# Kernel optimization log

Measured on AMD Instinct MI355X. Metric: run time of the kernel, lower is better.

Reference implementation:

```python
import jax, jax.numpy as jnp
import numpy as np

K = 3        # kernel_size
STRIDE = 1
PAD = 1


def _conv2d(x, w, stride, pad):
    return jax.lax.conv_general_dilated(
        x, w, window_strides=(stride, stride),
        padding=((pad, pad), (pad, pad)),
        dimension_numbers=("NCHW", "OIHW", "NCHW"))


def setup_inputs() -> dict:
    key = jax.random.key(0)
    k1, k2, k3, k4 = jax.random.split(key, 4)
    B, C, H, W = 8, 128, 56, 56
    OUT = 128
    x = jax.random.normal(k1, (B, C, H, W), jnp.float32)
    # small offset weights keep sampled coords mostly in-bounds (realistic trained regime)
    offset_w = jax.random.normal(k2, (2 * K * K, C, K, K), jnp.float32) * 0.01
    offset_b = jax.random.normal(k3, (2 * K * K,), jnp.float32) * 0.01
    conv_w = jax.random.normal(k4, (OUT, C, K, K), jnp.float32) * 0.02
    return {"x": x, "offset_w": offset_w, "offset_b": offset_b, "conv_w": conv_w}


def reference(x, offset_w, offset_b, conv_w):
    n = K * K
    # offset prediction conv (stride=STRIDE, padding=k//2) -> [b, 2n, h, w]
    offset = _conv2d(x, offset_w, STRIDE, K // 2) + offset_b[None, :, None, None]
    b, _, h, w = offset.shape
    # zero padding of the feature map
    xp = jnp.pad(x, ((0, 0), (0, 0), (PAD, PAD), (PAD, PAD)))
    c, Hp, Wp = xp.shape[1], xp.shape[2], xp.shape[3]

    # pn: fixed kernel offsets, y-first then x (matches torch.cat(y.flatten(), x.flatten()))
    r = jnp.arange(-(K // 2), K // 2 + 1, dtype=jnp.float32)
    py_n, px_n = jnp.meshgrid(r, r, indexing="ij")
    pn = jnp.concatenate([py_n.ravel(), px_n.ravel()])          # (2n,)

    # p0: kernel-center coordinates in padded map
    gy = jnp.arange(K // 2, h * STRIDE + 1, STRIDE, dtype=jnp.float32)
    gx = jnp.arange(K // 2, w * STRIDE + 1, STRIDE, dtype=jnp.float32)
    p0y, p0x = jnp.meshgrid(gy, gx, indexing="ij")               # (h, w)
    p0 = jnp.concatenate([jnp.broadcast_to(p0y, (n, h, w)),
                          jnp.broadcast_to(p0x, (n, h, w))], axis=0)[None]  # (1, 2n, h, w)

    p = p0 + pn[None, :, None, None] + offset                    # (b, 2n, h, w)
    p = jnp.transpose(p, (0, 2, 3, 1))                           # (b, h, w, 2n)

    q = jax.lax.stop_gradient(jnp.floor(p))                      # p.detach().floor()
    qlt_y = jnp.clip(q[..., :n], 0, Hp - 1)
    qlt_x = jnp.clip(q[..., n:], 0, Wp - 1)
    qrb_y = jnp.clip(q[..., :n] + 1, 0, Hp - 1)
    qrb_x = jnp.clip(q[..., n:] + 1, 0, Wp - 1)
    py = jnp.clip(p[..., :n], 0, Hp - 1)
    px = jnp.clip(p[..., n:], 0, Wp - 1)

    # bilinear weights; jnp.trunc reproduces the original's .long() truncation on one factor
    g_lt = (1 - (py - qlt_y)) * jnp.trunc(1 - (px - qlt_x))
    g_rb = (1 - (qrb_y - py)) * jnp.trunc(1 - (qrb_x - px))
    g_lb = (1 - (py - qlt_y)) * (1 - (qrb_x - px))               # q_lb = (qlt_y, qrb_x)
    g_rt = (1 - (qrb_y - py)) * (1 - (px - qlt_x))               # q_rt = (qrb_y, qlt_x)

    x_flat = xp.reshape(b, c, Hp * Wp)

    def gather(qy, qx):
        idx = (qy * Wp + qx).astype(jnp.int32).reshape(b, 1, -1)  # (b,1,h*w*n)
        out = jnp.take_along_axis(x_flat, jnp.broadcast_to(idx, (b, c, idx.shape[-1])), axis=-1)
        return out.reshape(b, c, h, w, n)

    x_off = (g_lt[:, None] * gather(qlt_y, qlt_x)
             + g_rb[:, None] * gather(qrb_y, qrb_x)
             + g_lb[:, None] * gather(qlt_y, qrb_x)
             + g_rt[:, None] * gather(qrb_y, qlt_x))             # (b, c, h, w, n)

    # tile each kxk sampled patch into a (h*k, w*k) map, matching _reshape_x_offset
    x_off = x_off.reshape(b, c, h, w, K, K).transpose(0, 1, 2, 4, 3, 5).reshape(b, c, h * K, w * K)

    # final conv: kernel k, stride k, no padding -> (b, out, h, w)
    return _conv2d(x_off, conv_w, K, 0)
```

## Files before the change

### kernel.cpp

```cpp
#include <hip/hip_runtime.h>
#include <cstdint>
#include <cstddef>

namespace {

constexpr int Bn   = 8;
constexpr int Cc   = 128;
constexpr int Hh   = 56;
constexpr int Ww   = 56;
constexpr int OUTC = 128;
constexpr int NTAP = 9;
constexpr int HW   = 3136;
constexpr int NPOS = Bn * HW;
constexpr int KDIM = 1152;
constexpr int CH   = Bn * 18 * HW;

constexpr int PT   = 32;
constexpr int CCH  = 64;
constexpr int KC   = CCH * NTAP;
constexpr int LROW = 584;

constexpr int OFFBLK = 1568;
constexpr int WBLK   = 576;

typedef __attribute__((ext_vector_type(8))) short  short8v;
typedef __attribute__((ext_vector_type(4))) short  short4v;
typedef __attribute__((ext_vector_type(4))) float  float4v;

__device__ __forceinline__ unsigned short f2bf(float f) {
    union { float f; uint32_t u; } v; v.f = f;
    const uint32_t u = v.u;
    return (unsigned short)((u + 0x7fffu + ((u >> 16) & 1u)) >> 16);
}
__device__ __forceinline__ float bf2f(unsigned short us) {
    union { uint32_t u; float f; } v; v.u = (uint32_t)us << 16;
    return v.f;
}

__global__ __launch_bounds__(256) void fused_prep_offset_kernel(
        const float* __restrict__ x, const float* __restrict__ ow,
        const float* __restrict__ cw,
        unsigned short* __restrict__ cwb, unsigned short* __restrict__ xt,
        float* __restrict__ partial) {
    __shared__ float red[4][64 * 18];

    const int blk = blockIdx.x;
    const int t   = threadIdx.x;

    if (blk >= OFFBLK) {
        const int pb = blk - OFFBLK;
        if (pb < WBLK) {
            const int i = pb * 256 + t;
            const int u   = i & 7;
            const int mq  = (i >> 3) & 63;
            const int wvv = (i >> 9) & 7;
            const int rest = i >> 12;
            const int ks = rest % 18, ccg = rest / 18;
            const int mm = mq >> 2, quad = mq & 3;
            const int klocal = ks * 32 + quad * 8 + u;
            const int n = klocal >> 6, cl = klocal & 63;
            const int o = wvv * 16 + mm;
            cwb[i] = f2bf(cw[o * KDIM + (ccg * CCH + cl) * NTAP + n]);
            return;
        }
        const int pb2 = pb - WBLK;
        const int b = pb2 & 7;
        const int ijb = (pb2 >> 3) * 64;
        const int lp2 = t & 63, cg = t >> 6;
        const float* xb = x + (size_t)b * Cc * HW + ijb + lp2;
#pragma unroll
        for (int c8 = 0; c8 < 4; ++c8) {
            short8v sv;
#pragma unroll
            for (int u = 0; u < 8; ++u)
                sv[u] = (short)f2bf(xb[(size_t)(cg * 32 + c8 * 8 + u) * HW]);
            const int g16 = cg * 4 + c8;
            *(short8v*)(xt + ((size_t)(b * 16 + g16) * HW + ijb + lp2) * 8) = sv;
        }
        return;
    }

    const int lane = t & 63;
    const int sq   = __builtin_amdgcn_readfirstlane(t >> 6);
    const int chunk = blk & 3;
    const int pgi  = blk >> 2;
    const int b    = pgi & 7;
    const int ijb  = (pgi >> 3) * 64;
    const int ij   = ijb + lane;
    const int i    = ij / Ww, j = ij % Ww;
    const float* xb = x + (size_t)b * Cc * HW;

    float acc[18];
#pragma unroll
    for (int m = 0; m < 18; ++m) acc[m] = 0.f;

    const int c0 = chunk * 32 + sq * 8;
    for (int cc = 0; cc < 8; ++cc) {
        const int c = c0 + cc;
        const float* xc = xb + (size_t)c * HW;
        float xv[9];
#pragma unroll
        for (int ky = 0; ky < 3; ++ky) {
            const int y = i + ky - 1;
            const bool yv = (unsigned)y < (unsigned)Hh;
#pragma unroll
            for (int kx = 0; kx < 3; ++kx) {
                const int xx = j + kx - 1;
                xv[ky * 3 + kx] = (yv && (unsigned)xx < (unsigned)Ww) ? xc[y * Ww + xx] : 0.f;
            }
        }
        const float* wc = ow + c * NTAP;
#pragma unroll
        for (int m = 0; m < 18; ++m) {
#pragma unroll
            for (int tap = 0; tap < 9; ++tap)
                acc[m] = fmaf(wc[m * KDIM + tap], xv[tap], acc[m]);
        }
    }

#pragma unroll
    for (int m = 0; m < 18; ++m) red[sq][lane * 18 + m] = acc[m];
    __syncthreads();

    float* pout = partial + (size_t)chunk * CH;
    for (int e = t; e < 64 * 18; e += 256) {
        const int lpe = e / 18, m = e % 18;
        const float s01 = red[0][e] + red[1][e];
        const float s23 = red[2][e] + red[3][e];
        pout[(size_t)(b * 18 + m) * HW + ijb + lpe] = s01 + s23;
    }
}

__global__ __launch_bounds__(512, 6) void deform_mfma_kernel(
        const unsigned short* __restrict__ xt, const unsigned short* __restrict__ cwb,
        const float* __restrict__ partial, const float* __restrict__ ob,
        float* __restrict__ out) {
    __shared__ unsigned short xoffB[PT * LROW];
    __shared__ float4v pgS[PT * NTAP];
    __shared__ int2    poS[PT * NTAP];

    const int t    = threadIdx.x;
    const int lane = t & 63;
    const int mm   = lane & 15, quad = lane >> 4;
    const int wv   = t >> 6;
    const int lp   = t & 31;
    const int grp  = (t >> 5) & 7;
    const int nh   = t >> 8;
    const int blk  = blockIdx.x;
    const int b    = blk & 7;
    const int ijb  = (blk >> 3) * PT;
    const unsigned short* xtb = xt + (size_t)b * 16 * HW * 8;

    for (int e = t; e < PT * NTAP; e += 512) {
        const int n = e >> 5, lpe = e & 31;
        const int ij = ijb + lpe;
        const size_t iy = (size_t)(b * 18 + n) * HW + ij;
        const size_t ix = (size_t)(b * 18 + 9 + n) * HW + ij;
        float sy = (partial[iy] + partial[CH + iy]) + (partial[2 * CH + iy] + partial[3 * CH + iy]);
        float sx = (partial[ix] + partial[CH + ix]) + (partial[2 * CH + ix] + partial[3 * CH + ix]);
        sy = sy + ob[n];
        sx = sx + ob[9 + n];
        const float py = (float)(ij / Ww + n / 3) + sy;
        const float px = (float)(ij % Ww + n % 3) + sx;
        const float q0y = floorf(py), q0x = floorf(px);
        const float lty = fminf(fmaxf(q0y, 0.f), 57.f);
        const float ltx = fminf(fmaxf(q0x, 0.f), 57.f);
        const float rby = fminf(fmaxf(q0y + 1.f, 0.f), 57.f);
        const float rbx = fminf(fmaxf(q0x + 1.f, 0.f), 57.f);
        const float pyc = fminf(fmaxf(py, 0.f), 57.f);
        const float pxc = fminf(fmaxf(px, 0.f), 57.f);
        float g0 = (1.f - (pyc - lty)) * truncf(1.f - (pxc - ltx));
        float g1 = (1.f - (rby - pyc)) * truncf(1.f - (rbx - pxc));
        float g2 = (1.f - (pyc - lty)) * (1.f - (rbx - pxc));
        float g3 = (1.f - (rby - pyc)) * (1.f - (pxc - ltx));
        const int y0 = (int)lty - 1, x0 = (int)ltx - 1;
        const int y1 = (int)rby - 1, x1 = (int)rbx - 1;
        const bool v0y = (unsigned)y0 < (unsigned)Hh, v0x = (unsigned)x0 < (unsigned)Ww;
        const bool v1y = (unsigned)y1 < (unsigned)Hh, v1x = (unsigned)x1 < (unsigned)Ww;
        int o0 = y0 * Ww + x0, o1 = y1 * Ww + x1, o2 = y0 * Ww + x1, o3 = y1 * Ww + x0;
        if (!(v0y && v0x)) { o0 = 0; g0 = 0.f; }
        if (!(v1y && v1x)) { o1 = 0; g1 = 0.f; }
        if (!(v0y && v1x)) { o2 = 0; g2 = 0.f; }
        if (!(v1y && v0x)) { o3 = 0; g3 = 0.f; }
        pgS[e] = (float4v){ g2, g3, g0, g1 };
        poS[e] = make_int2((o2 & 0xffff) | (o3 << 16), (o0 & 0xffff) | (o1 << 16));
    }

    float4v acc[2] = { {0.f,0.f,0.f,0.f}, {0.f,0.f,0.f,0.f} };
    __syncthreads();

    for (int cc = 0; cc < 2; ++cc) {
        if (cc) __syncthreads();
        const unsigned short* pl = xtb + (size_t)(cc * 8 + grp) * HW * 8;
#pragma unroll
        for (int nn = 0; nn < 5; ++nn) {
            const int n = nn * 2 + nh;
            if (n < 9) {
                const float4v G = pgS[n * 32 + lp];
                const int2  O = poS[n * 32 + lp];
                const short8v a0 = *(const short8v*)(pl + (size_t)(O.y & 0xffff) * 8);
                const short8v a2 = *(const short8v*)(pl + (size_t)(O.x & 0xffff) * 8);
                const short8v a3 = *(const short8v*)(pl + (size_t)((O.x >> 16) & 0xffff) * 8);
                const short8v a1 = *(const short8v*)(pl + (size_t)((O.y >> 16) & 0xffff) * 8);
                short8v sv;
#pragma unroll
                for (int u = 0; u < 8; ++u) {
                    float v = G.x * bf2f((unsigned short)a2[u]);
                    v = fmaf(G.y, bf2f((unsigned short)a3[u]), v);
                    v = fmaf(G.z, bf2f((unsigned short)a0[u]), v);
                    v = fmaf(G.w, bf2f((unsigned short)a1[u]), v);
                    sv[u] = (short)f2bf(v);
                }
                *(short8v*)&xoffB[lp * LROW + n * CCH + grp * 8] = sv;
            }
        }
        __syncthreads();

        const unsigned short* bw = cwb + (size_t)(cc * 144 + wv) * 512 + (mm * 4 + quad) * 8;
        const unsigned short* ap0 = &xoffB[mm * LROW + quad * 8];
#pragma unroll 3
        for (int ks = 0; ks < KC / 32; ++ks) {
            const int kl = ks * 32;
            const short8v b0 = *(const short8v*)(bw + ks * 4096);
#pragma unroll
            for (int pt = 0; pt < 2; ++pt) {
                const unsigned short* ap = ap0 + pt * 16 * LROW + kl;
                const short4v alo = *(const short4v*)ap;
                const short4v ahi = *(const short4v*)(ap + 4);
                const short8v a = __builtin_shufflevector(alo, ahi, 0, 1, 2, 3, 4, 5, 6, 7);
                acc[pt] = __builtin_amdgcn_mfma_f32_16x16x32_bf16(a, b0, acc[pt], 0, 0, 0);
            }
        }
    }

    float* ob0 = out + (size_t)(b * OUTC + wv * 16 + mm) * HW + ijb + quad * 4;
#pragma unroll
    for (int pt = 0; pt < 2; ++pt)
        *(float4v*)(ob0 + pt * 16) = acc[pt];
}

}

extern "C" void kernel_launch(void* const* d_in, const int* in_sizes, int n_in,
                              void* d_out, int out_size, void* d_ws, size_t ws_size,
                              hipStream_t stream) {
    const float* x  = (const float*)d_in[0];
    const float* ow = (const float*)d_in[1];
    const float* ob = (const float*)d_in[2];
    const float* cw = (const float*)d_in[3];
    float* out = (float*)d_out;

    char* wsp = (char*)d_ws;
    unsigned short* cwb = (unsigned short*)wsp;
    unsigned short* xt = (unsigned short*)(wsp + 294912);
    float* partial = (float*)(wsp + 6717440);

    fused_prep_offset_kernel<<<OFFBLK + WBLK + 392, 256, 0, stream>>>(
        x, ow, cw, cwb, xt, partial);
    deform_mfma_kernel<<<NPOS / PT, 512, 0, stream>>>(xt, cwb, partial, ob, out);
}
```

Measured before the change: 127.8 us.

## Merge prep and deform kernels into one persistent cooperative kernel with grid sync

Replaces the two launches with a single cooperative persistent kernel. Each 512-thread block processes two 256-thread prep units per round (offset conv partials, weight bf16 repack, x transpose), then all blocks meet at a grid-wide sync before looping over the deform/MFMA output tiles. The goal is to remove the second launch and the gap between kernels. In exchange it adds a grid barrier, shared-memory aliasing, fewer resident blocks (grid capped at 768) and a redundant duplicate store of each output tile.

```diff
diff --git a/kernel.cpp b/kernel.cpp
--- a/kernel.cpp
+++ b/kernel.cpp
@@ -1,6 +1,9 @@
 #include <hip/hip_runtime.h>
+#include <hip/hip_cooperative_groups.h>
 #include <cstdint>
 #include <cstddef>
+
+namespace cg = cooperative_groups;
 
 namespace {
 
@@ -15,13 +18,15 @@
 constexpr int KDIM = 1152;
 constexpr int CH   = Bn * 18 * HW;
 
-constexpr int PT   = 32;
-constexpr int CCH  = 64;
-constexpr int KC   = CCH * NTAP;
-constexpr int LROW = 584;
+constexpr int PT    = 32;
+constexpr int CCH   = 64;
+constexpr int KC    = CCH * NTAP;
+constexpr int LROW  = 584;
+constexpr int NTILE = NPOS / PT;
 
 constexpr int OFFBLK = 1568;
 constexpr int WBLK   = 576;
+constexpr int NUNIT  = 2536;
 
 typedef __attribute__((ext_vector_type(8))) short  short8v;
 typedef __attribute__((ext_vector_type(4))) short  short4v;
@@ -37,206 +42,222 @@
     return v.f;
 }
 
-__global__ __launch_bounds__(256) void fused_prep_offset_kernel(
+__global__ __launch_bounds__(512, 6) void deform_all(
         const float* __restrict__ x, const float* __restrict__ ow,
-        const float* __restrict__ cw,
+        const float* __restrict__ ob, const float* __restrict__ cw,
         unsigned short* __restrict__ cwb, unsigned short* __restrict__ xt,
-        float* __restrict__ partial) {
-    __shared__ float red[4][64 * 18];
-
+        float* __restrict__ partial, float* __restrict__ out) {
+    __shared__ __align__(16) char smem[44288];
+    const int t   = threadIdx.x;
     const int blk = blockIdx.x;
-    const int t   = threadIdx.x;
-
-    if (blk >= OFFBLK) {
-        const int pb = blk - OFFBLK;
-        if (pb < WBLK) {
-            const int i = pb * 256 + t;
-            const int u   = i & 7;
-            const int mq  = (i >> 3) & 63;
-            const int wvv = (i >> 9) & 7;
-            const int rest = i >> 12;
-            const int ks = rest % 18, ccg = rest / 18;
-            const int mm = mq >> 2, quad = mq & 3;
-            const int klocal = ks * 32 + quad * 8 + u;
-            const int n = klocal >> 6, cl = klocal & 63;
-            const int o = wvv * 16 + mm;
-            cwb[i] = f2bf(cw[o * KDIM + (ccg * CCH + cl) * NTAP + n]);
-            return;
-        }
-        const int pb2 = pb - WBLK;
-        const int b = pb2 & 7;
-        const int ijb = (pb2 >> 3) * 64;
-        const int lp2 = t & 63, cg = t >> 6;
-        const float* xb = x + (size_t)b * Cc * HW + ijb + lp2;
-#pragma unroll
-        for (int c8 = 0; c8 < 4; ++c8) {
-            short8v sv;
-#pragma unroll
-            for (int u = 0; u < 8; ++u)
-                sv[u] = (short)f2bf(xb[(size_t)(cg * 32 + c8 * 8 + u) * HW]);
-            const int g16 = cg * 4 + c8;
-            *(short8v*)(xt + ((size_t)(b * 16 + g16) * HW + ijb + lp2) * 8) = sv;
-        }
-        return;
+    const int g   = gridDim.x;
+
+    {
+        const int h  = t >> 8;
+        const int t2 = t & 255;
+        float* redh = (float*)smem + h * 4608;
+        const int slots  = g * 2;
+        const int rounds = (NUNIT + slots - 1) / slots;
+        for (int r = 0; r < rounds; ++r) {
+            const int vu = r * slots + 2 * blk + h;
+            const bool isoff = (vu < OFFBLK);
+            if (isoff) {
+                const int lane = t2 & 63;
+                const int sq   = __builtin_amdgcn_readfirstlane(t2 >> 6);
+                const int chunk = vu & 3;
+                const int pgi  = vu >> 2;
+                const int b    = pgi & 7;
+                const int ijb  = (pgi >> 3) * 64;
+                const int ij   = ijb + lane;
+                const int i    = ij / Ww, j = ij % Ww;
+                const float* xb = x + (size_t)b * Cc * HW;
+                float acc[18];
+#pragma unroll
+                for (int m = 0; m < 18; ++m) acc[m] = 0.f;
+                const int c0 = chunk * 32 + sq * 8;
+                for (int ccl = 0; ccl < 8; ++ccl) {
+                    const int c = c0 + ccl;
+                    const float* xc = xb + (size_t)c * HW;
+                    float xv[9];
+#pragma unroll
+                    for (int ky = 0; ky < 3; ++ky) {
+                        const int y = i + ky - 1;
+                        const bool yv = (unsigned)y < (unsigned)Hh;
+#pragma unroll
+                        for (int kx = 0; kx < 3; ++kx) {
+                            const int xx = j + kx - 1;
+                            xv[ky * 3 + kx] = (yv && (unsigned)xx < (unsigned)Ww) ? xc[y * Ww + xx] : 0.f;
+                        }
+                    }
+                    const float* wc = ow + c * NTAP;
+#pragma unroll
+                    for (int m = 0; m < 18; ++m) {
+#pragma unroll
+                        for (int tap = 0; tap < 9; ++tap)
+                            acc[m] = fmaf(wc[m * KDIM + tap], xv[tap], acc[m]);
+                    }
+                }
+#pragma unroll
+                for (int m = 0; m < 18; ++m) redh[sq * 1152 + lane * 18 + m] = acc[m];
+            } else if (vu < OFFBLK + WBLK) {
+                const int i = (vu - OFFBLK) * 256 + t2;
+                const int u   = i & 7;
+                const int mq  = (i >> 3) & 63;
+                const int wvv = (i >> 9) & 7;
+                const int rest = i >> 12;
+                const int ks = rest % 18, ccg = rest / 18;
+                const int mmw = mq >> 2, quadw = mq & 3;
+                const int klocal = ks * 32 + quadw * 8 + u;
+                const int n = klocal >> 6, cl = klocal & 63;
+                const int o = wvv * 16 + mmw;
+                cwb[i] = f2bf(cw[o * KDIM + (ccg * CCH + cl) * NTAP + n]);
+            } else if (vu < NUNIT) {
+                const int pb2 = vu - (OFFBLK + WBLK);
+                const int b = pb2 & 7;
+                const int ijb = (pb2 >> 3) * 64;
+                const int lp2 = t2 & 63, cgi = t2 >> 6;
+                const float* xb = x + (size_t)b * Cc * HW + ijb + lp2;
+#pragma unroll
+                for (int c8 = 0; c8 < 4; ++c8) {
+                    short8v sv;
+#pragma unroll
+                    for (int u = 0; u < 8; ++u)
+                        sv[u] = (short)f2bf(xb[(size_t)(cgi * 32 + c8 * 8 + u) * HW]);
+                    const int g16 = cgi * 4 + c8;
+                    *(short8v*)(xt + ((size_t)(b * 16 + g16) * HW + ijb + lp2) * 8) = sv;
+                }
+            }
+            __syncthreads();
+            if (isoff) {
+                const int chunk = vu & 3;
+                const int pgi = vu >> 2;
+                const int b = pgi & 7;
+                const int ijb = (pgi >> 3) * 64;
+                float* pout = partial + (size_t)chunk * CH;
+                for (int e = t2; e < 1152; e += 256) {
+                    const int lpe = e / 18, m = e % 18;
+                    const float s01 = redh[e] + redh[1152 + e];
+                    const float s23 = redh[2304 + e] + redh[3456 + e];
+                    pout[(size_t)(b * 18 + m) * HW + ijb + lpe] = s01 + s23;
+                }
+            }
+            __syncthreads();
+        }
     }
 
-    const int lane = t & 63;
-    const int sq   = __builtin_amdgcn_readfirstlane(t >> 6);
-    const int chunk = blk & 3;
-    const int pgi  = blk >> 2;
-    const int b    = pgi & 7;
-    const int ijb  = (pgi >> 3) * 64;
-    const int ij   = ijb + lane;
-    const int i    = ij / Ww, j = ij % Ww;
-    const float* xb = x + (size_t)b * Cc * HW;
-
-    float acc[18];
-#pragma unroll
-    for (int m = 0; m < 18; ++m) acc[m] = 0.f;
-
-    const int c0 = chunk * 32 + sq * 8;
-    for (int cc = 0; cc < 8; ++cc) {
-        const int c = c0 + cc;
-        const float* xc = xb + (size_t)c * HW;
-        float xv[9];
-#pragma unroll
-        for (int ky = 0; ky < 3; ++ky) {
-            const int y = i + ky - 1;
-            const bool yv = (unsigned)y < (unsigned)Hh;
-#pragma unroll
-            for (int kx = 0; kx < 3; ++kx) {
-                const int xx = j + kx - 1;
-                xv[ky * 3 + kx] = (yv && (unsigned)xx < (unsigned)Ww) ? xc[y * Ww + xx] : 0.f;
-            }
-        }
-        const float* wc = ow + c * NTAP;
-#pragma unroll
-        for (int m = 0; m < 18; ++m) {
-#pragma unroll
-            for (int tap = 0; tap < 9; ++tap)
-                acc[m] = fmaf(wc[m * KDIM + tap], xv[tap], acc[m]);
-        }
-    }
-
-#pragma unroll
-    for (int m = 0; m < 18; ++m) red[sq][lane * 18 + m] = acc[m];
-    __syncthreads();
-
-    float* pout = partial + (size_t)chunk * CH;
-    for (int e = t; e < 64 * 18; e += 256) {
-        const int lpe = e / 18, m = e % 18;
-        const float s01 = red[0][e] + red[1][e];
-        const float s23 = red[2][e] + red[3][e];
-        pout[(size_t)(b * 18 + m) * HW + ijb + lpe] = s01 + s23;
-    }
-}
-
-__global__ __launch_bounds__(512, 6) void deform_mfma_kernel(
-        const unsigned short* __restrict__ xt, const unsigned short* __restrict__ cwb,
-        const float* __restrict__ partial, const float* __restrict__ ob,
-        float* __restrict__ out) {
-    __shared__ unsigned short xoffB[PT * LROW];
-    __shared__ float4v pgS[PT * NTAP];
-    __shared__ int2    poS[PT * NTAP];
-
-    const int t    = threadIdx.x;
+    __threadfence();
+    cg::this_grid().sync();
+
+    unsigned short* xoffB = (unsigned short*)smem;
+    float4v* pgS = (float4v*)(smem + 37376);
+    int2*    poS = (int2*)(smem + 37376 + 4608);
+
     const int lane = t & 63;
     const int mm   = lane & 15, quad = lane >> 4;
     const int wv   = t >> 6;
     const int lp   = t & 31;
     const int grp  = (t >> 5) & 7;
     const int nh   = t >> 8;
-    const int blk  = blockIdx.x;
-    const int b    = blk & 7;
-    const int ijb  = (blk >> 3) * PT;
-    const unsigned short* xtb = xt + (size_t)b * 16 * HW * 8;
-
-    for (int e = t; e < PT * NTAP; e += 512) {
-        const int n = e >> 5, lpe = e & 31;
-        const int ij = ijb + lpe;
-        const size_t iy = (size_t)(b * 18 + n) * HW + ij;
-        const size_t ix = (size_t)(b * 18 + 9 + n) * HW + ij;
-        float sy = (partial[iy] + partial[CH + iy]) + (partial[2 * CH + iy] + partial[3 * CH + iy]);
-        float sx = (partial[ix] + partial[CH + ix]) + (partial[2 * CH + ix] + partial[3 * CH + ix]);
-        sy = sy + ob[n];
-        sx = sx + ob[9 + n];
-        const float py = (float)(ij / Ww + n / 3) + sy;
-        const float px = (float)(ij % Ww + n % 3) + sx;
-        const float q0y = floorf(py), q0x = floorf(px);
-        const float lty = fminf(fmaxf(q0y, 0.f), 57.f);
-        const float ltx = fminf(fmaxf(q0x, 0.f), 57.f);
-        const float rby = fminf(fmaxf(q0y + 1.f, 0.f), 57.f);
-        const float rbx = fminf(fmaxf(q0x + 1.f, 0.f), 57.f);
-        const float pyc = fminf(fmaxf(py, 0.f), 57.f);
-        const float pxc = fminf(fmaxf(px, 0.f), 57.f);
-        float g0 = (1.f - (pyc - lty)) * truncf(1.f - (pxc - ltx));
-        float g1 = (1.f - (rby - pyc)) * truncf(1.f - (rbx - pxc));
-        float g2 = (1.f - (pyc - lty)) * (1.f - (rbx - pxc));
-        float g3 = (1.f - (rby - pyc)) * (1.f - (pxc - ltx));
-        const int y0 = (int)lty - 1, x0 = (int)ltx - 1;
-        const int y1 = (int)rby - 1, x1 = (int)rbx - 1;
-        const bool v0y = (unsigned)y0 < (unsigned)Hh, v0x = (unsigned)x0 < (unsigned)Ww;
-        const bool v1y = (unsigned)y1 < (unsigned)Hh, v1x = (unsigned)x1 < (unsigned)Ww;
-        int o0 = y0 * Ww + x0, o1 = y1 * Ww + x1, o2 = y0 * Ww + x1, o3 = y1 * Ww + x0;
-        if (!(v0y && v0x)) { o0 = 0; g0 = 0.f; }
-        if (!(v1y && v1x)) { o1 = 0; g1 = 0.f; }
-        if (!(v0y && v1x)) { o2 = 0; g2 = 0.f; }
-        if (!(v1y && v0x)) { o3 = 0; g3 = 0.f; }
-        pgS[e] = (float4v){ g2, g3, g0, g1 };
-        poS[e] = make_int2((o2 & 0xffff) | (o3 << 16), (o0 & 0xffff) | (o1 << 16));
+    const unsigned short* xtB = xt;
+
+    for (int base = 0; base < NTILE; base += g) {
+        const int w = (NTILE - base < g) ? (NTILE - base) : g;
+        const int off = blk - (g - w);
+        if (off < 0) continue;
+        const int ti  = base + off;
+        const int b   = ti & 7;
+        const int ijb = (ti >> 3) * PT;
+        const unsigned short* xtb = xtB + (size_t)b * 16 * HW * 8;
+
+        for (int e = t; e < PT * NTAP; e += 512) {
+            const int n = e >> 5, lpe = e & 31;
+            const int ij = ijb + lpe;
+            const size_t iy = (size_t)(b * 18 + n) * HW + ij;
+            const size_t ix = (size_t)(b * 18 + 9 + n) * HW + ij;
+            float sy = (partial[iy] + partial[CH + iy]) + (partial[2 * CH + iy] + partial[3 * CH + iy]);
+            float sx = (partial[ix] + partial[CH + ix]) + (partial[2 * CH + ix] + partial[3 * CH + ix]);
+            sy = sy + ob[n];
+            sx = sx + ob[9 + n];
+            const float py = (float)(ij / Ww + n / 3) + sy;
+            const float px = (float)(ij % Ww + n % 3) + sx;
+            const float q0y = floorf(py), q0x = floorf(px);
+            const float lty = fminf(fmaxf(q0y, 0.f), 57.f);
+            const float ltx = fminf(fmaxf(q0x, 0.f), 57.f);
+            const float rby = fminf(fmaxf(q0y + 1.f, 0.f), 57.f);
+            const float rbx = fminf(fmaxf(q0x + 1.f, 0.f), 57.f);
+            const float pyc = fminf(fmaxf(py, 0.f), 57.f);
+            const float pxc = fminf(fmaxf(px, 0.f), 57.f);
+            float g0 = (1.f - (pyc - lty)) * truncf(1.f - (pxc - ltx));
+            float g1 = (1.f - (rby - pyc)) * truncf(1.f - (rbx - pxc));
+            float g2 = (1.f - (pyc - lty)) * (1.f - (rbx - pxc));
+            float g3 = (1.f - (rby - pyc)) * (1.f - (pxc - ltx));
+            const int y0 = (int)lty - 1, x0 = (int)ltx - 1;
+            const int y1 = (int)rby - 1, x1 = (int)rbx - 1;
+            const bool v0y = (unsigned)y0 < (unsigned)Hh, v0x = (unsigned)x0 < (unsigned)Ww;
+            const bool v1y = (unsigned)y1 < (unsigned)Hh, v1x = (unsigned)x1 < (unsigned)Ww;
+            int o0 = y0 * Ww + x0, o1 = y1 * Ww + x1, o2 = y0 * Ww + x1, o3 = y1 * Ww + x0;
+            if (!(v0y && v0x)) { o0 = 0; g0 = 0.f; }
+            if (!(v1y && v1x)) { o1 = 0; g1 = 0.f; }
+            if (!(v0y && v1x)) { o2 = 0; g2 = 0.f; }
+            if (!(v1y && v0x)) { o3 = 0; g3 = 0.f; }
+            pgS[e] = (float4v){ g2, g3, g0, g1 };
+            poS[e] = make_int2((o2 & 0xffff) | (o3 << 16), (o0 & 0xffff) | (o1 << 16));
+        }
+
+        float4v acc[2] = { {0.f,0.f,0.f,0.f}, {0.f,0.f,0.f,0.f} };
+        __syncthreads();
+
+        for (int cc = 0; cc < 2; ++cc) {
+            if (cc) __syncthreads();
+            const unsigned short* pl = xtb + (size_t)(cc * 8 + grp) * HW * 8;
+#pragma unroll
+            for (int nn = 0; nn < 5; ++nn) {
+                const int n = nn * 2 + nh;
+                if (n < 9) {
+                    const float4v G = pgS[n * 32 + lp];
+                    const int2  O = poS[n * 32 + lp];
+                    const short8v a0 = *(const short8v*)(pl + (size_t)(O.y & 0xffff) * 8);
+                    const short8v a2 = *(const short8v*)(pl + (size_t)(O.x & 0xffff) * 8);
+                    const short8v a3 = *(const short8v*)(pl + (size_t)((O.x >> 16) & 0xffff) * 8);
+                    const short8v a1 = *(const short8v*)(pl + (size_t)((O.y >> 16) & 0xffff) * 8);
+                    short8v sv;
+#pragma unroll
+                    for (int u = 0; u < 8; ++u) {
+                        float v = G.x * bf2f((unsigned short)a2[u]);
+                        v = fmaf(G.y, bf2f((unsigned short)a3[u]), v);
+                        v = fmaf(G.z, bf2f((unsigned short)a0[u]), v);
+                        v = fmaf(G.w, bf2f((unsigned short)a1[u]), v);
+                        sv[u] = (short)f2bf(v);
+                    }
+                    *(short8v*)&xoffB[lp * LROW + n * CCH + grp * 8] = sv;
+                }
+            }
+            __syncthreads();
+
+            const unsigned short* bw = cwb + (size_t)(cc * 144 + wv) * 512 + (mm * 4 + quad) * 8;
+            const unsigned short* ap0 = &xoffB[mm * LROW + quad * 8];
+#pragma unroll 3
+            for (int ks = 0; ks < KC / 32; ++ks) {
+                const int kl = ks * 32;
+                const short8v b0 = *(const short8v*)(bw + ks * 4096);
+#pragma unroll
+                for (int pt = 0; pt < 2; ++pt) {
+                    const unsigned short* ap = ap0 + pt * 16 * LROW + kl;
+                    const short4v alo = *(const short4v*)ap;
+                    const short4v ahi = *(const short4v*)(ap + 4);
+                    const short8v a = __builtin_shufflevector(alo, ahi, 0, 1, 2, 3, 4, 5, 6, 7);
+                    acc[pt] = __builtin_amdgcn_mfma_f32_16x16x32_bf16(a, b0, acc[pt], 0, 0, 0);
+                }
+            }
+        }
+
+        float* ob0 = out + (size_t)(b * OUTC + wv * 16 + mm) * HW + ijb + quad * 4;
+#pragma unroll
+        for (int pt = 0; pt < 2; ++pt) {
+            *(float4v*)(ob0 + pt * 16) = acc[pt];
+            *(float4v*)(ob0 + (size_t)0 * HW + pt * 16) = acc[pt];
+        }
     }
-
-    float4v acc[2] = { {0.f,0.f,0.f,0.f}, {0.f,0.f,0.f,0.f} };
-    __syncthreads();
-
-    for (int cc = 0; cc < 2; ++cc) {
-        if (cc) __syncthreads();
-        const unsigned short* pl = xtb + (size_t)(cc * 8 + grp) * HW * 8;
-#pragma unroll
-        for (int nn = 0; nn < 5; ++nn) {
-            const int n = nn * 2 + nh;
-            if (n < 9) {
-                const float4v G = pgS[n * 32 + lp];
-                const int2  O = poS[n * 32 + lp];
-                const short8v a0 = *(const short8v*)(pl + (size_t)(O.y & 0xffff) * 8);
-                const short8v a2 = *(const short8v*)(pl + (size_t)(O.x & 0xffff) * 8);
-                const short8v a3 = *(const short8v*)(pl + (size_t)((O.x >> 16) & 0xffff) * 8);
-                const short8v a1 = *(const short8v*)(pl + (size_t)((O.y >> 16) & 0xffff) * 8);
-                short8v sv;
-#pragma unroll
-                for (int u = 0; u < 8; ++u) {
-                    float v = G.x * bf2f((unsigned short)a2[u]);
-                    v = fmaf(G.y, bf2f((unsigned short)a3[u]), v);
-                    v = fmaf(G.z, bf2f((unsigned short)a0[u]), v);
-                    v = fmaf(G.w, bf2f((unsigned short)a1[u]), v);
-                    sv[u] = (short)f2bf(v);
-                }
-                *(short8v*)&xoffB[lp * LROW + n * CCH + grp * 8] = sv;
-            }
-        }
-        __syncthreads();
-
-        const unsigned short* bw = cwb + (size_t)(cc * 144 + wv) * 512 + (mm * 4 + quad) * 8;
-        const unsigned short* ap0 = &xoffB[mm * LROW + quad * 8];
-#pragma unroll 3
-        for (int ks = 0; ks < KC / 32; ++ks) {
-            const int kl = ks * 32;
-            const short8v b0 = *(const short8v*)(bw + ks * 4096);
-#pragma unroll
-            for (int pt = 0; pt < 2; ++pt) {
-                const unsigned short* ap = ap0 + pt * 16 * LROW + kl;
-                const short4v alo = *(const short4v*)ap;
-                const short4v ahi = *(const short4v*)(ap + 4);
-                const short8v a = __builtin_shufflevector(alo, ahi, 0, 1, 2, 3, 4, 5, 6, 7);
-                acc[pt] = __builtin_amdgcn_mfma_f32_16x16x32_bf16(a, b0, acc[pt], 0, 0, 0);
-            }
-        }
-    }
-
-    float* ob0 = out + (size_t)(b * OUTC + wv * 16 + mm) * HW + ijb + quad * 4;
-#pragma unroll
-    for (int pt = 0; pt < 2; ++pt)
-        *(float4v*)(ob0 + pt * 16) = acc[pt];
 }
 
 }
@@ -255,7 +276,17 @@
     unsigned short* xt = (unsigned short*)(wsp + 294912);
     float* partial = (float*)(wsp + 6717440);
 
-    fused_prep_offset_kernel<<<OFFBLK + WBLK + 392, 256, 0, stream>>>(
-        x, ow, cw, cwb, xt, partial);
-    deform_mfma_kernel<<<NPOS / PT, 512, 0, stream>>>(xt, cwb, partial, ob, out);
-}
+    static int gridn = -1;
+    if (gridn < 0) {
+        int nb = 0;
+        if (hipOccupancyMaxActiveBlocksPerMultiprocessor(&nb, deform_all, 512, 0) != hipSuccess || nb < 1)
+            nb = 1;
+        gridn = nb * 256;
+        if (gridn > 768) gridn = 768;
+    }
+
+    void* args[] = { (void*)&x, (void*)&ow, (void*)&ob, (void*)&cw,
+                     (void*)&cwb, (void*)&xt, (void*)&partial, (void*)&out };
+    hipLaunchCooperativeKernel((const void*)deform_all, dim3(gridn), dim3(512),
+                               args, 0, stream);
+}
```

Result: slower. 271.6 us (+112.6%).
